# Kernel optimization log

Hardware: AMD Instinct MI355X
Metric: run time of the kernel (lower is better)

Reference implementation:

```python
import jax, jax.numpy as jnp
import numpy as np


def _pairwise_sqdist(a, b):
    # a: [m, n, d], b: [m, n, d] -> M: [m, n, n], M[m,i,j] = ||a[m,i]-b[m,j]||^2
    # Use the expansion |a|^2 + |b|^2 - 2 a.b to avoid materializing the
    # [m, n, n, d] difference tensor; clamp tiny negatives from cancellation.
    a2 = jnp.sum(a * a, axis=-1)  # [m, n]
    b2 = jnp.sum(b * b, axis=-1)  # [m, n]
    ab = jnp.einsum('mid,mjd->mij', a, b)  # [m, n, n]
    return jnp.maximum(a2[:, :, None] + b2[:, None, :] - 2.0 * ab, 0.0)


def setup_inputs() -> dict:
    key = jax.random.key(0)
    k1, k2 = jax.random.split(key)
    template = jax.random.normal(k1, (16, 4096, 3), dtype=jnp.float32)
    source = jax.random.normal(k2, (16, 4096, 3), dtype=jnp.float32)
    return {"template": template, "source": source}


def reference(template, source):
    M = _pairwise_sqdist(template, source)  # [m, n, n]
    # min over template index (axis 1): nearest template point for each source point
    dist1 = jnp.mean(jnp.sqrt(jnp.min(M, axis=1)))
    # min over source index (axis 2): nearest source point for each template point
    dist2 = jnp.mean(jnp.sqrt(jnp.min(M, axis=2)))
    return (dist1 + dist2) / 2.0
```

## Files before the change

kernel.cpp:

```cpp
#include <hip/hip_runtime.h>

#define N_PTS   4096
#define N_BATCH 16
#define INV_CNT (1.0f / (2.0f * N_BATCH * N_PTS))
#define AROW_BYTES ((size_t)2 * N_BATCH * N_PTS * 16 * 2)
#define NQUERY (2 * N_BATCH * N_PTS)
#define NFBLK  128

typedef _Float16 f16x8  __attribute__((ext_vector_type(8)));
#define AS1 __attribute__((address_space(1)))
#define AS3 __attribute__((address_space(3)))

__global__ __launch_bounds__(256) void prep_kernel(
    const float* __restrict__ tpl, const float* __restrict__ src,
    _Float16* __restrict__ arow, float* __restrict__ out) {
    int pt = blockIdx.x * 256 + threadIdx.x;
    if (pt == 0) out[0] = 0.0f;
    const float* p = (pt < 65536 ? tpl : src) + (size_t)(pt & 65535) * 3;
    float x = p[0], y = p[1], z = p[2];
    float o2 = fmaf(x, x, fmaf(y, y, z * z));
    _Float16 xh = (_Float16)x, yh = (_Float16)y, zh = (_Float16)z;
    _Float16 xl = (_Float16)(x - (float)xh);
    _Float16 yl = (_Float16)(y - (float)yh);
    _Float16 zl = (_Float16)(z - (float)zh);
    _Float16 o2h = (_Float16)o2;
    _Float16 o2l = (_Float16)(o2 - (float)o2h);
    const _Float16 m2 = (_Float16)-2.0f;
    f16x8 v0, v1;
    v0[0] = m2 * xh; v0[1] = m2 * yh; v0[2] = m2 * zh;
    v0[3] = m2 * xl; v0[4] = m2 * yl; v0[5] = m2 * zl;
    v0[6] = m2 * xh; v0[7] = m2 * yh;
    v1[0] = m2 * zh; v1[1] = o2h; v1[2] = o2l;
    v1[3] = (_Float16)0.0f; v1[4] = (_Float16)0.0f; v1[5] = (_Float16)0.0f;
    v1[6] = (_Float16)0.0f; v1[7] = (_Float16)0.0f;
    *(f16x8*)(arow + (size_t)pt * 16)     = v0;
    *(f16x8*)(arow + (size_t)pt * 16 + 8) = v1;
}

#define FD(a,x,y) "v_min3_f32 %[" #a "], v" #x ", v" #y ", %[" #a "]\n\t"
#define FOLD_A FD(acc0,32,33) FD(acc1,34,35) FD(acc0,36,37) FD(acc1,38,39) \
               FD(acc0,40,41) FD(acc1,42,43) FD(acc0,44,45) FD(acc1,46,47) \
               FD(acc2,64,65) FD(acc3,66,67) FD(acc2,68,69) FD(acc3,70,71) \
               FD(acc2,72,73) FD(acc3,74,75) FD(acc2,76,77) FD(acc3,78,79)
#define FOLD_B FD(acc0,48,49) FD(acc1,50,51) FD(acc0,52,53) FD(acc1,54,55) \
               FD(acc0,56,57) FD(acc1,58,59) FD(acc0,60,61) FD(acc1,62,63) \
               FD(acc2,80,81) FD(acc3,82,83) FD(acc2,84,85) FD(acc3,86,87) \
               FD(acc2,88,89) FD(acc3,90,91) FD(acc2,92,93) FD(acc3,94,95)
#define MF_A(d) \
  "v_mfma_f32_32x32x16_f16 v[32:47], %[" #d "], %[bf0], v[96:111]\n\t" \
  "v_mfma_f32_32x32x16_f16 v[64:79], %[" #d "], %[bf1], v[96:111]\n\t"
#define MF_B(d) \
  "v_mfma_f32_32x32x16_f16 v[48:63], %[" #d "], %[bf0], v[96:111]\n\t" \
  "v_mfma_f32_32x32x16_f16 v[80:95], %[" #d "], %[bf1], v[96:111]\n\t"
#define DSR(d,off) "ds_read_b128 %[" #d "], %[dsa] offset:" #off "\n\t"
#define WL(n) "s_waitcnt lgkmcnt(" #n ")\n\t"
#define ZM(r) "v_mov_b32 v" #r ", 0\n\t"
#define NOP3 "s_nop 7\n\t" "s_nop 7\n\t" "s_nop 7\n\t"

__global__ __launch_bounds__(256, 3) void chamfer_mfma(
    const float* __restrict__ tpl, const float* __restrict__ src,
    const _Float16* __restrict__ arow, float* __restrict__ qmin) {
    __shared__ uint4 sbuf[2][1024];

    const int tid = threadIdx.x;
    const int wv = tid >> 6, lane = tid & 63;
    const int n = lane & 31, g = lane >> 5;
    const int lin = blockIdx.x + 16 * (blockIdx.y + 16 * blockIdx.z);
    const int wgid  = (lin & 7) * 128 + (lin >> 3);
    const int qb    = wgid & 15;
    const int batch = (wgid >> 4) & 15;
    const int dh    = wgid >> 8;
    const int dir   = dh >> 1;
    const int ahalf = dh & 1;

    const float* qpts = (dir == 0) ? src : tpl;
    const _Float16* abase = arow + ((dir == 0) ? (size_t)0 : (size_t)65536 * 16)
                          + (size_t)batch * 4096 * 16
                          + (size_t)ahalf * 2048 * 16;

    f16x8 bfr[2];
    float p2[2];
    #pragma unroll
    for (int i = 0; i < 2; ++i) {
        const int q = qb * 256 + wv * 64 + i * 32 + n;
        const float* p = qpts + (size_t)(batch * 4096 + q) * 3;
        float px = p[0], py = p[1], pz = p[2];
        p2[i] = fmaf(px, px, fmaf(py, py, pz * pz));
        _Float16 xh = (_Float16)px, yh = (_Float16)py, zh = (_Float16)pz;
        _Float16 xl = (_Float16)(px - (float)xh);
        _Float16 yl = (_Float16)(py - (float)yh);
        _Float16 zl = (_Float16)(pz - (float)zh);
        f16x8 b;
        if (g == 0) {
            b[0] = xh; b[1] = yh; b[2] = zh;
            b[3] = xh; b[4] = yh; b[5] = zh;
            b[6] = xl; b[7] = yl;
        } else {
            b[0] = zl; b[1] = (_Float16)1.0f; b[2] = (_Float16)1.0f;
            b[3] = (_Float16)0.0f; b[4] = (_Float16)0.0f; b[5] = (_Float16)0.0f;
            b[6] = (_Float16)0.0f; b[7] = (_Float16)0.0f;
        }
        bfr[i] = b;
    }

    const int lane_off = n * 32 + g * 16;
    const unsigned dsa0 = (unsigned)(size_t)((AS3 char*)&sbuf[0][0]) + lane_off;

    const char* gwave = (const char*)abase + wv * 4096 + lane * 16;
    #define STAGE(ch)                                                          \
        {                                                                      \
            const char* gp = gwave + (size_t)(ch) * 16384;                     \
            AS3 char* lp = (AS3 char*)&sbuf[(ch) & 1][0] + wv * 4096;          \
            _Pragma("unroll")                                                  \
            for (int j = 0; j < 4; ++j)                                        \
                __builtin_amdgcn_global_load_lds(                              \
                    (const AS1 unsigned*)(gp + j * 1024),                      \
                    (AS3 unsigned*)(lp + j * 1024), 16, 0, 0);                 \
        }

    float acc0 = 1e30f, acc1 = 1e30f, acc2 = 1e30f, acc3 = 1e30f;
    f16x8 d0, d1, d2, d3;

    STAGE(0)
    #pragma unroll 1
    for (int c = 0; c < 4; ++c) {
        if (c < 3) STAGE(c + 1)
        if (c < 3)
            asm volatile("s_waitcnt vmcnt(4)\n\ts_barrier" ::: "memory");
        else
            asm volatile("s_waitcnt vmcnt(0)\n\ts_barrier" ::: "memory");
        const unsigned dsa = dsa0 + ((unsigned)(c & 1) << 14);

        asm volatile(
            ZM(96) ZM(97) ZM(98) ZM(99) ZM(100) ZM(101) ZM(102) ZM(103)
            ZM(104) ZM(105) ZM(106) ZM(107) ZM(108) ZM(109) ZM(110) ZM(111)
            DSR(d0,0) DSR(d1,1024) DSR(d2,2048) DSR(d3,3072)
            WL(3) MF_A(d0) DSR(d0,4096) NOP3
            WL(3) MF_B(d1) DSR(d1,5120)  FOLD_A
            WL(3) MF_A(d2) DSR(d2,6144)  FOLD_B
            WL(3) MF_B(d3) DSR(d3,7168)  FOLD_A
            WL(3) MF_A(d0) DSR(d0,8192)  FOLD_B
            WL(3) MF_B(d1) DSR(d1,9216)  FOLD_A
            WL(3) MF_A(d2) DSR(d2,10240) FOLD_B
            WL(3) MF_B(d3) DSR(d3,11264) FOLD_A
            WL(3) MF_A(d0) DSR(d0,12288) FOLD_B
            WL(3) MF_B(d1) DSR(d1,13312) FOLD_A
            WL(3) MF_A(d2) DSR(d2,14336) FOLD_B
            WL(3) MF_B(d3) DSR(d3,15360) FOLD_A
            WL(3) MF_A(d0) FOLD_B
            WL(2) MF_B(d1) FOLD_A
            WL(1) MF_A(d2) FOLD_B
            WL(0) MF_B(d3) FOLD_A
            NOP3 FOLD_B
            : [d0]"=&v"(d0), [d1]"=&v"(d1), [d2]"=&v"(d2), [d3]"=&v"(d3),
              [acc0]"+v"(acc0), [acc1]"+v"(acc1),
              [acc2]"+v"(acc2), [acc3]"+v"(acc3)
            : [bf0]"v"(bfr[0]), [bf1]"v"(bfr[1]), [dsa]"v"(dsa)
            : "memory",
              "v32","v33","v34","v35","v36","v37","v38","v39",
              "v40","v41","v42","v43","v44","v45","v46","v47",
              "v48","v49","v50","v51","v52","v53","v54","v55",
              "v56","v57","v58","v59","v60","v61","v62","v63",
              "v64","v65","v66","v67","v68","v69","v70","v71",
              "v72","v73","v74","v75","v76","v77","v78","v79",
              "v80","v81","v82","v83","v84","v85","v86","v87",
              "v88","v89","v90","v91","v92","v93","v94","v95",
              "v96","v97","v98","v99","v100","v101","v102","v103",
              "v104","v105","v106","v107","v108","v109","v110","v111");

        asm volatile("s_barrier" ::: "memory");
    }

    float v0 = fminf(acc0, acc1);
    v0 = fminf(v0, __shfl_xor(v0, 32));
    float v1 = fminf(acc2, acc3);
    v1 = fminf(v1, __shfl_xor(v1, 32));
    float dd0 = fmaxf(v0 + p2[0], 0.0f);
    float dd1 = fmaxf(v1 + p2[1], 0.0f);
    if (g == 0) {
        const int qid = ((dir * N_BATCH + batch) << 12) + qb * 256 + wv * 64 + n;
        qmin[(size_t)ahalf * NQUERY + qid]      = dd0;
        qmin[(size_t)ahalf * NQUERY + qid + 32] = dd1;
    }
}

__global__ __launch_bounds__(256) void final_kernel(
    const float* __restrict__ qmin, float* __restrict__ out) {
    __shared__ float wsum[4];
    float s = 0.0f;
    const int base = blockIdx.x * (NQUERY / NFBLK) + threadIdx.x;
    #pragma unroll
    for (int j = 0; j < NQUERY / NFBLK / 256; ++j) {
        const int q = base + j * 256;
        s += sqrtf(fminf(qmin[q], qmin[NQUERY + q]));
    }
    s *= INV_CNT;
    #pragma unroll
    for (int off = 32; off > 0; off >>= 1) s += __shfl_down(s, off);
    if ((threadIdx.x & 63) == 0) wsum[threadIdx.x >> 6] = s;
    __syncthreads();
    if (threadIdx.x == 0)
        atomicAdd(out, wsum[0] + wsum[1] + wsum[2] + wsum[3]);
}

extern "C" void kernel_launch(void* const* d_in, const int* in_sizes, int n_in,
                              void* d_out, int out_size, void* d_ws, size_t ws_size,
                              hipStream_t stream) {
    const float* tpl = (const float*)d_in[0];
    const float* src = (const float*)d_in[1];
    float* out = (float*)d_out;
    _Float16* arow = (_Float16*)d_ws;
    float* qmin = (float*)((char*)d_ws + AROW_BYTES);
    (void)in_sizes; (void)n_in; (void)out_size; (void)ws_size;

    hipLaunchKernelGGL(prep_kernel, dim3((2 * N_BATCH * N_PTS) / 256),
                       dim3(256), 0, stream, tpl, src, arow, out);
    dim3 grid(N_PTS / 256, N_BATCH, 4);
    hipLaunchKernelGGL(chamfer_mfma, grid, dim3(256), 0, stream,
                       tpl, src, arow, qmin);
    hipLaunchKernelGGL(final_kernel, dim3(NFBLK), dim3(256), 0, stream,
                       qmin, out);
}
```

Measured before the change: 77.68 us.

## Double queries per wave to reuse each LDS A-fragment across four MFMAs

Each wave now handles 128 query points (four B fragments) instead of 64, so every LDS-loaded reference fragment feeds four MFMAs instead of two. LDS read traffic and staging per query fall by half and the grid shrinks to 512 workgroups. The block-to-region mapping is reworked to match. The cost is about 176 VGPRs, so occupancy drops to 2 blocks per CU, and the fewer blocks may fill the CUs less evenly.

```diff
diff --git a/kernel.cpp b/kernel.cpp
--- a/kernel.cpp
+++ b/kernel.cpp
@@ -38,26 +38,40 @@
 }
 
 #define FD(a,x,y) "v_min3_f32 %[" #a "], v" #x ", v" #y ", %[" #a "]\n\t"
-#define FOLD_A FD(acc0,32,33) FD(acc1,34,35) FD(acc0,36,37) FD(acc1,38,39) \
-               FD(acc0,40,41) FD(acc1,42,43) FD(acc0,44,45) FD(acc1,46,47) \
-               FD(acc2,64,65) FD(acc3,66,67) FD(acc2,68,69) FD(acc3,70,71) \
-               FD(acc2,72,73) FD(acc3,74,75) FD(acc2,76,77) FD(acc3,78,79)
-#define FOLD_B FD(acc0,48,49) FD(acc1,50,51) FD(acc0,52,53) FD(acc1,54,55) \
-               FD(acc0,56,57) FD(acc1,58,59) FD(acc0,60,61) FD(acc1,62,63) \
-               FD(acc2,80,81) FD(acc3,82,83) FD(acc2,84,85) FD(acc3,86,87) \
-               FD(acc2,88,89) FD(acc3,90,91) FD(acc2,92,93) FD(acc3,94,95)
-#define MF_A(d) \
-  "v_mfma_f32_32x32x16_f16 v[32:47], %[" #d "], %[bf0], v[96:111]\n\t" \
-  "v_mfma_f32_32x32x16_f16 v[64:79], %[" #d "], %[bf1], v[96:111]\n\t"
-#define MF_B(d) \
-  "v_mfma_f32_32x32x16_f16 v[48:63], %[" #d "], %[bf0], v[96:111]\n\t" \
-  "v_mfma_f32_32x32x16_f16 v[80:95], %[" #d "], %[bf1], v[96:111]\n\t"
+#define FOLD_P0 \
+  FD(acc0,32,33) FD(acc1,34,35) FD(acc0,36,37) FD(acc1,38,39) \
+  FD(acc0,40,41) FD(acc1,42,43) FD(acc0,44,45) FD(acc1,46,47) \
+  FD(acc2,48,49) FD(acc3,50,51) FD(acc2,52,53) FD(acc3,54,55) \
+  FD(acc2,56,57) FD(acc3,58,59) FD(acc2,60,61) FD(acc3,62,63) \
+  FD(acc4,64,65) FD(acc5,66,67) FD(acc4,68,69) FD(acc5,70,71) \
+  FD(acc4,72,73) FD(acc5,74,75) FD(acc4,76,77) FD(acc5,78,79) \
+  FD(acc6,80,81) FD(acc7,82,83) FD(acc6,84,85) FD(acc7,86,87) \
+  FD(acc6,88,89) FD(acc7,90,91) FD(acc6,92,93) FD(acc7,94,95)
+#define FOLD_P1 \
+  FD(acc0,96,97)   FD(acc1,98,99)   FD(acc0,100,101) FD(acc1,102,103) \
+  FD(acc0,104,105) FD(acc1,106,107) FD(acc0,108,109) FD(acc1,110,111) \
+  FD(acc2,112,113) FD(acc3,114,115) FD(acc2,116,117) FD(acc3,118,119) \
+  FD(acc2,120,121) FD(acc3,122,123) FD(acc2,124,125) FD(acc3,126,127) \
+  FD(acc4,128,129) FD(acc5,130,131) FD(acc4,132,133) FD(acc5,134,135) \
+  FD(acc4,136,137) FD(acc5,138,139) FD(acc4,140,141) FD(acc5,142,143) \
+  FD(acc6,144,145) FD(acc7,146,147) FD(acc6,148,149) FD(acc7,150,151) \
+  FD(acc6,152,153) FD(acc7,154,155) FD(acc6,156,157) FD(acc7,158,159)
+#define MFP0(d) \
+  "v_mfma_f32_32x32x16_f16 v[32:47],   %[" #d "], %[bf0], v[160:175]\n\t" \
+  "v_mfma_f32_32x32x16_f16 v[48:63],   %[" #d "], %[bf1], v[160:175]\n\t" \
+  "v_mfma_f32_32x32x16_f16 v[64:79],   %[" #d "], %[bf2], v[160:175]\n\t" \
+  "v_mfma_f32_32x32x16_f16 v[80:95],   %[" #d "], %[bf3], v[160:175]\n\t"
+#define MFP1(d) \
+  "v_mfma_f32_32x32x16_f16 v[96:111],  %[" #d "], %[bf0], v[160:175]\n\t" \
+  "v_mfma_f32_32x32x16_f16 v[112:127], %[" #d "], %[bf1], v[160:175]\n\t" \
+  "v_mfma_f32_32x32x16_f16 v[128:143], %[" #d "], %[bf2], v[160:175]\n\t" \
+  "v_mfma_f32_32x32x16_f16 v[144:159], %[" #d "], %[bf3], v[160:175]\n\t"
 #define DSR(d,off) "ds_read_b128 %[" #d "], %[dsa] offset:" #off "\n\t"
 #define WL(n) "s_waitcnt lgkmcnt(" #n ")\n\t"
 #define ZM(r) "v_mov_b32 v" #r ", 0\n\t"
 #define NOP3 "s_nop 7\n\t" "s_nop 7\n\t" "s_nop 7\n\t"
 
-__global__ __launch_bounds__(256, 3) void chamfer_mfma(
+__global__ __launch_bounds__(256, 2) void chamfer_mfma(
     const float* __restrict__ tpl, const float* __restrict__ src,
     const _Float16* __restrict__ arow, float* __restrict__ qmin) {
     __shared__ uint4 sbuf[2][1024];
@@ -65,24 +79,25 @@
     const int tid = threadIdx.x;
     const int wv = tid >> 6, lane = tid & 63;
     const int n = lane & 31, g = lane >> 5;
-    const int lin = blockIdx.x + 16 * (blockIdx.y + 16 * blockIdx.z);
-    const int wgid  = (lin & 7) * 128 + (lin >> 3);
-    const int qb    = wgid & 15;
-    const int batch = (wgid >> 4) & 15;
-    const int dh    = wgid >> 8;
-    const int dir   = dh >> 1;
-    const int ahalf = dh & 1;
+    const int lin = blockIdx.x + 8 * (blockIdx.y + 16 * blockIdx.z);
+    const int s_  = lin >> 3;
+    const int qb  = s_ & 7;
+    const int region = (lin & 7) + 8 * (s_ >> 3);
+    const int batch  = region & 15;
+    const int dh     = region >> 4;
+    const int dir    = dh >> 1;
+    const int ahalf  = dh & 1;
 
     const float* qpts = (dir == 0) ? src : tpl;
     const _Float16* abase = arow + ((dir == 0) ? (size_t)0 : (size_t)65536 * 16)
                           + (size_t)batch * 4096 * 16
                           + (size_t)ahalf * 2048 * 16;
 
-    f16x8 bfr[2];
-    float p2[2];
+    f16x8 bfr[4];
+    float p2[4];
     #pragma unroll
-    for (int i = 0; i < 2; ++i) {
-        const int q = qb * 256 + wv * 64 + i * 32 + n;
+    for (int i = 0; i < 4; ++i) {
+        const int q = qb * 512 + wv * 128 + i * 32 + n;
         const float* p = qpts + (size_t)(batch * 4096 + q) * 3;
         float px = p[0], py = p[1], pz = p[2];
         p2[i] = fmaf(px, px, fmaf(py, py, pz * pz));
@@ -119,43 +134,48 @@
         }
 
     float acc0 = 1e30f, acc1 = 1e30f, acc2 = 1e30f, acc3 = 1e30f;
+    float acc4 = 1e30f, acc5 = 1e30f, acc6 = 1e30f, acc7 = 1e30f;
     f16x8 d0, d1, d2, d3;
 
     STAGE(0)
     #pragma unroll 1
     for (int c = 0; c < 4; ++c) {
-        if (c < 3) STAGE(c + 1)
-        if (c < 3)
+        if (c < 3) {
+            STAGE(c + 1)
             asm volatile("s_waitcnt vmcnt(4)\n\ts_barrier" ::: "memory");
-        else
+        } else {
             asm volatile("s_waitcnt vmcnt(0)\n\ts_barrier" ::: "memory");
+        }
         const unsigned dsa = dsa0 + ((unsigned)(c & 1) << 14);
 
         asm volatile(
-            ZM(96) ZM(97) ZM(98) ZM(99) ZM(100) ZM(101) ZM(102) ZM(103)
-            ZM(104) ZM(105) ZM(106) ZM(107) ZM(108) ZM(109) ZM(110) ZM(111)
+            ZM(160) ZM(161) ZM(162) ZM(163) ZM(164) ZM(165) ZM(166) ZM(167)
+            ZM(168) ZM(169) ZM(170) ZM(171) ZM(172) ZM(173) ZM(174) ZM(175)
             DSR(d0,0) DSR(d1,1024) DSR(d2,2048) DSR(d3,3072)
-            WL(3) MF_A(d0) DSR(d0,4096) NOP3
-            WL(3) MF_B(d1) DSR(d1,5120)  FOLD_A
-            WL(3) MF_A(d2) DSR(d2,6144)  FOLD_B
-            WL(3) MF_B(d3) DSR(d3,7168)  FOLD_A
-            WL(3) MF_A(d0) DSR(d0,8192)  FOLD_B
-            WL(3) MF_B(d1) DSR(d1,9216)  FOLD_A
-            WL(3) MF_A(d2) DSR(d2,10240) FOLD_B
-            WL(3) MF_B(d3) DSR(d3,11264) FOLD_A
-            WL(3) MF_A(d0) DSR(d0,12288) FOLD_B
-            WL(3) MF_B(d1) DSR(d1,13312) FOLD_A
-            WL(3) MF_A(d2) DSR(d2,14336) FOLD_B
-            WL(3) MF_B(d3) DSR(d3,15360) FOLD_A
-            WL(3) MF_A(d0) FOLD_B
-            WL(2) MF_B(d1) FOLD_A
-            WL(1) MF_A(d2) FOLD_B
-            WL(0) MF_B(d3) FOLD_A
-            NOP3 FOLD_B
+            WL(3) MFP0(d0) DSR(d0,4096)
+            WL(3) MFP1(d1) DSR(d1,5120)  FOLD_P0
+            WL(3) MFP0(d2) DSR(d2,6144)  FOLD_P1
+            WL(3) MFP1(d3) DSR(d3,7168)  FOLD_P0
+            WL(3) MFP0(d0) DSR(d0,8192)  FOLD_P1
+            WL(3) MFP1(d1) DSR(d1,9216)  FOLD_P0
+            WL(3) MFP0(d2) DSR(d2,10240) FOLD_P1
+            WL(3) MFP1(d3) DSR(d3,11264) FOLD_P0
+            WL(3) MFP0(d0) DSR(d0,12288) FOLD_P1
+            WL(3) MFP1(d1) DSR(d1,13312) FOLD_P0
+            WL(3) MFP0(d2) DSR(d2,14336) FOLD_P1
+            WL(3) MFP1(d3) DSR(d3,15360) FOLD_P0
+            WL(3) MFP0(d0) FOLD_P1
+            WL(2) MFP1(d1) FOLD_P0
+            WL(1) MFP0(d2) FOLD_P1
+            WL(0) MFP1(d3) FOLD_P0
+            NOP3 FOLD_P1
             : [d0]"=&v"(d0), [d1]"=&v"(d1), [d2]"=&v"(d2), [d3]"=&v"(d3),
               [acc0]"+v"(acc0), [acc1]"+v"(acc1),
-              [acc2]"+v"(acc2), [acc3]"+v"(acc3)
-            : [bf0]"v"(bfr[0]), [bf1]"v"(bfr[1]), [dsa]"v"(dsa)
+              [acc2]"+v"(acc2), [acc3]"+v"(acc3),
+              [acc4]"+v"(acc4), [acc5]"+v"(acc5),
+              [acc6]"+v"(acc6), [acc7]"+v"(acc7)
+            : [bf0]"v"(bfr[0]), [bf1]"v"(bfr[1]), [bf2]"v"(bfr[2]),
+              [bf3]"v"(bfr[3]), [dsa]"v"(dsa)
             : "memory",
               "v32","v33","v34","v35","v36","v37","v38","v39",
               "v40","v41","v42","v43","v44","v45","v46","v47",
@@ -166,21 +186,30 @@
               "v80","v81","v82","v83","v84","v85","v86","v87",
               "v88","v89","v90","v91","v92","v93","v94","v95",
               "v96","v97","v98","v99","v100","v101","v102","v103",
-              "v104","v105","v106","v107","v108","v109","v110","v111");
+              "v104","v105","v106","v107","v108","v109","v110","v111",
+              "v112","v113","v114","v115","v116","v117","v118","v119",
+              "v120","v121","v122","v123","v124","v125","v126","v127",
+              "v128","v129","v130","v131","v132","v133","v134","v135",
+              "v136","v137","v138","v139","v140","v141","v142","v143",
+              "v144","v145","v146","v147","v148","v149","v150","v151",
+              "v152","v153","v154","v155","v156","v157","v158","v159",
+              "v160","v161","v162","v163","v164","v165","v166","v167",
+              "v168","v169","v170","v171","v172","v173","v174","v175");
 
         asm volatile("s_barrier" ::: "memory");
     }
 
-    float v0 = fminf(acc0, acc1);
-    v0 = fminf(v0, __shfl_xor(v0, 32));
-    float v1 = fminf(acc2, acc3);
-    v1 = fminf(v1, __shfl_xor(v1, 32));
-    float dd0 = fmaxf(v0 + p2[0], 0.0f);
-    float dd1 = fmaxf(v1 + p2[1], 0.0f);
+    float m0 = fminf(acc0, acc1);  m0 = fminf(m0, __shfl_xor(m0, 32));
+    float m1 = fminf(acc2, acc3);  m1 = fminf(m1, __shfl_xor(m1, 32));
+    float m2 = fminf(acc4, acc5);  m2 = fminf(m2, __shfl_xor(m2, 32));
+    float m3 = fminf(acc6, acc7);  m3 = fminf(m3, __shfl_xor(m3, 32));
     if (g == 0) {
-        const int qid = ((dir * N_BATCH + batch) << 12) + qb * 256 + wv * 64 + n;
-        qmin[(size_t)ahalf * NQUERY + qid]      = dd0;
-        qmin[(size_t)ahalf * NQUERY + qid + 32] = dd1;
+        const int qid = ((dir * N_BATCH + batch) << 12) + qb * 512 + wv * 128 + n;
+        float* qp = qmin + (size_t)ahalf * NQUERY + qid;
+        qp[0]  = fmaxf(m0 + p2[0], 0.0f);
+        qp[32] = fmaxf(m1 + p2[1], 0.0f);
+        qp[64] = fmaxf(m2 + p2[2], 0.0f);
+        qp[96] = fmaxf(m3 + p2[3], 0.0f);
     }
 }
 
@@ -215,7 +244,7 @@
 
     hipLaunchKernelGGL(prep_kernel, dim3((2 * N_BATCH * N_PTS) / 256),
                        dim3(256), 0, stream, tpl, src, arow, out);
-    dim3 grid(N_PTS / 256, N_BATCH, 4);
+    dim3 grid(8, N_BATCH, 4);
     hipLaunchKernelGGL(chamfer_mfma, grid, dim3(256), 0, stream,
                        tpl, src, arow, qmin);
     hipLaunchKernelGGL(final_kernel, dim3(NFBLK), dim3(256), 0, stream,
```

Result: no change. 77.23 us (-0.6%).
